# Performance work log

Hardware: AMD Instinct MI355X
Metric: run time of the kernel (lower is better)

## Reference

```python
import jax, jax.numpy as jnp
import numpy as np

N, E, F_IN, H, D = 50000, 800000, 128, 4, 32


def setup_inputs() -> dict:
    key = jax.random.key(0)
    k_x, k_e, k_w, k_al, k_ar = jax.random.split(key, 5)
    x = jax.random.normal(k_x, (N, F_IN), dtype=jnp.float32)
    edge_index = jax.random.randint(k_e, (2, E), 0, N, dtype=jnp.int32).astype(jnp.int64)
    # xavier-uniform-like scales
    s_w = float(np.sqrt(6.0 / (F_IN + H * D)))
    s_a = float(np.sqrt(6.0 / (D + 1)))
    W = jax.random.uniform(k_w, (F_IN, H * D), jnp.float32, -s_w, s_w)
    att_l = jax.random.uniform(k_al, (H, D), jnp.float32, -s_a, s_a)
    att_r = jax.random.uniform(k_ar, (H, D), jnp.float32, -s_a, s_a)
    bias = jnp.zeros((H * D,), jnp.float32)
    return {"x": x, "edge_index": edge_index, "W": W, "att_l": att_l, "att_r": att_r, "bias": bias}


def reference(x, edge_index, W, att_l, att_r, bias):
    num_nodes = x.shape[0]
    n_heads, head_dim = att_l.shape
    h = (x @ W).reshape(num_nodes, n_heads, head_dim)          # [N,H,D]
    alpha_l = jnp.einsum('nhd,hd->nh', h, att_l)               # [N,H]
    alpha_r = jnp.einsum('nhd,hd->nh', h, att_r)               # [N,H]
    from_idx, to_idx = edge_index[0], edge_index[1]
    att = alpha_l[from_idx] + alpha_r[to_idx]                  # [E,H]
    att = jax.nn.leaky_relu(att, negative_slope=0.2)
    # segment softmax over edges grouped by destination node (shift by global
    # per-head max, exactly as the source's _softmax effectively does)
    att = att - jax.lax.stop_gradient(jnp.max(att, axis=0, keepdims=True))
    ex = jnp.exp(att)                                          # [E,H]
    denom = jax.ops.segment_sum(ex, to_idx, num_segments=num_nodes)  # [N,H]
    att_n = ex / (denom[to_idx] + 1e-9)                        # [E,H]
    # scatter-weighted aggregation: out[n] = sum_{e: to=n} att[e] * h[from[e]]
    msgs = att_n[:, :, None] * h[from_idx]                     # [E,H,D]
    out = jax.ops.segment_sum(msgs, to_idx, num_segments=num_nodes)  # [N,H,D]
    out = out.reshape(num_nodes, n_heads * head_dim) + bias
    return out
```

## Files before the change

kernel.cpp:

```cpp
#include <hip/hip_runtime.h>
#include <cstdint>

#define N_NODES 50000
#define N_EDGES 800000
#define F_IN    128
#define N_HEADS 4
#define HEAD_DIM 32
#define F_OUT   128

#define NBUCK   391
#define NPB     128
#define KA_GRID 256
#define EPB     (N_EDGES / KA_GRID)
#define CAPA    32
#define REC_CAP 2560
#define STAGE_CAP REC_CAP
#define NSTRIP  (N_NODES / 16)
#define NGEMM   ((NSTRIP + 3) / 4)

typedef unsigned int uint32;
typedef unsigned short ushort;
typedef __attribute__((ext_vector_type(8))) short short8v;
typedef __attribute__((ext_vector_type(4))) float float4v;

typedef __attribute__((address_space(1))) const float gfloat;
typedef __attribute__((address_space(3))) float lfloat;

__device__ __forceinline__ ushort f2bf(float f) {
    uint32 u = __float_as_uint(f);
    return (ushort)((u + 0x7FFFu + ((u >> 16) & 1u)) >> 16);
}


__device__ __forceinline__ int block_scan_excl_256(int v, int* p_total)
{
    const int t = threadIdx.x, lane = t & 63, wv = t >> 6;
    int incl = v;
#pragma unroll
    for (int d = 1; d < 64; d <<= 1) {
        int u = __shfl_up(incl, d);
        if (lane >= d) incl += u;
    }
    __shared__ int wsum[4];
    if (lane == 63) wsum[wv] = incl;
    __syncthreads();
    int woff = 0;
#pragma unroll
    for (int j = 0; j < 4; ++j) {
        int s = wsum[j];
        if (j < wv) woff += s;
    }
    if (p_total) *p_total = wsum[0] + wsum[1] + wsum[2] + wsum[3];
    __syncthreads();
    return woff + incl - v;
}

__global__ __launch_bounds__(256) void k_prep(const float* __restrict__ W,
    ushort* __restrict__ WT_hi, ushort* __restrict__ WT_lo)
{
    const int id = blockIdx.x * 256 + threadIdx.x;
    if (id < F_IN * F_OUT) {
        const int n = id & 127, k = id >> 7;
        const float w = W[k * F_OUT + n];
        const ushort hi = f2bf(w);
        const float hif = __uint_as_float((uint32)hi << 16);
        WT_hi[n * F_IN + k] = hi;
        WT_lo[n * F_IN + k] = f2bf(w - hif);
    }
}

__global__ __launch_bounds__(256, 4) void k_bin_gemm(
    const int* __restrict__ ei, const float* __restrict__ x,
    const ushort* __restrict__ WT_hi, const ushort* __restrict__ WT_lo,
    const float* __restrict__ attl, const float* __restrict__ attr,
    uint2* __restrict__ priv, int* __restrict__ cnts,
    uint32* __restrict__ hbq, float* __restrict__ aLp, float* __restrict__ aRp)
{
    __shared__ float xl[4][16 * 128];
    __shared__ int cur[NBUCK];

    if (blockIdx.x < KA_GRID) {
        const int sb = blockIdx.x, t = threadIdx.x;
        for (int bb = t; bb < NBUCK; bb += 256) cur[bb] = 0;
        __syncthreads();
        const int e0 = sb * EPB;
        for (int i = t; i < EPB; i += 256) {
            const int from = ei[e0 + i];
            const int to   = ei[N_EDGES + e0 + i];
            const int b = to >> 7;
            const int slot = atomicAdd(&cur[b], 1);
            if (slot < CAPA)
                priv[((size_t)b * KA_GRID + sb) * CAPA + slot] =
                    make_uint2((uint32)from, (uint32)to);
        }
        __syncthreads();
        for (int bb = t; bb < NBUCK; bb += 256)
            cnts[sb * NBUCK + bb] = min(cur[bb], CAPA);
        return;
    }

    const int bid   = blockIdx.x - KA_GRID;
    const int lane  = threadIdx.x & 63;
    const int wv    = threadIdx.x >> 6;
    const int strip = bid * 4 + wv;
    if (strip >= NSTRIP) return;
    const int q     = lane >> 4;
    const int c15   = lane & 15;
    const int row0  = strip * 16;

    const float* gbase = x + (size_t)row0 * F_IN;
    float* lbase = &xl[wv][0];
#pragma unroll
    for (int i = 0; i < 8; ++i) {
        __builtin_amdgcn_global_load_lds(
            (gfloat*)(gbase + i * 256 + lane * 4),
            (lfloat*)(lbase + i * 256), 16, 0, 0);
    }
    __asm volatile("s_waitcnt vmcnt(0)" ::: "memory");

    const float* arow = lbase + c15 * F_IN + q * 8;
    short8v ahi[4], alo[4];
#pragma unroll
    for (int kt = 0; kt < 4; ++kt) {
        const float4 f0 = *(const float4*)(arow + kt * 32);
        const float4 f1 = *(const float4*)(arow + kt * 32 + 4);
        const float fs[8] = {f0.x, f0.y, f0.z, f0.w, f1.x, f1.y, f1.z, f1.w};
#pragma unroll
        for (int j = 0; j < 8; ++j) {
            const ushort hi = f2bf(fs[j]);
            const float hif = __uint_as_float((uint32)hi << 16);
            ahi[kt][j] = (short)hi;
            alo[kt][j] = (short)f2bf(fs[j] - hif);
        }
    }

    float4v acc[8];
#pragma unroll
    for (int nt = 0; nt < 8; ++nt) {
        float4v a = {0.f, 0.f, 0.f, 0.f};
        const ushort* bhb = WT_hi + ((nt * 16 + c15) << 7) + q * 8;
        const ushort* blb = WT_lo + ((nt * 16 + c15) << 7) + q * 8;
#pragma unroll
        for (int kt = 0; kt < 4; ++kt) {
            const short8v bh = *(const short8v*)(bhb + kt * 32);
            const short8v bl = *(const short8v*)(blb + kt * 32);
            a = __builtin_amdgcn_mfma_f32_16x16x32_bf16(ahi[kt], bh, a, 0, 0, 0);
            a = __builtin_amdgcn_mfma_f32_16x16x32_bf16(alo[kt], bh, a, 0, 0, 0);
            a = __builtin_amdgcn_mfma_f32_16x16x32_bf16(ahi[kt], bl, a, 0, 0, 0);
        }
        acc[nt] = a;
    }

#pragma unroll
    for (int nt = 0; nt < 4; ++nt) {
#pragma unroll
        for (int r = 0; r < 4; ++r) {
            const uint32 d = (uint32)f2bf(acc[nt][r]) | ((uint32)f2bf(acc[nt + 4][r]) << 16);
            hbq[(size_t)(row0 + q * 4 + r) * 64 + nt * 16 + c15] = d;
        }
    }

    float aLacc[4][4] = {{0.f}}, aRacc[4][4] = {{0.f}};
#pragma unroll
    for (int nt = 0; nt < 8; ++nt) {
        const float alv = attl[nt * 16 + c15];
        const float arv = attr[nt * 16 + c15];
        const int hh = nt >> 1;
#pragma unroll
        for (int r = 0; r < 4; ++r) {
            aLacc[r][hh] = fmaf(acc[nt][r], alv, aLacc[r][hh]);
            aRacc[r][hh] = fmaf(acc[nt][r], arv, aRacc[r][hh]);
        }
    }
#pragma unroll
    for (int r = 0; r < 4; ++r) {
#pragma unroll
        for (int hh = 0; hh < 4; ++hh) {
            float vl = aLacc[r][hh], vr = aRacc[r][hh];
#pragma unroll
            for (int d = 1; d < 16; d <<= 1) {
                vl += __shfl_xor(vl, d);
                vr += __shfl_xor(vr, d);
            }
            if (c15 == hh) {
                const int row = row0 + q * 4 + r;
                const int pos = (hh & 1) * 2 + (hh >> 1);
                aLp[row * N_HEADS + pos] = vl;
                aRp[row * N_HEADS + pos] = vr;
            }
        }
    }
}

__global__ __launch_bounds__(256) void k_build(const uint2* __restrict__ priv,
    const int* __restrict__ cnts,
    int* __restrict__ count, int* __restrict__ offsets, int* __restrict__ rec_from)
{
    __shared__ uint2 stage[STAGE_CAP];
    __shared__ int so_s[256], cts_s[256];
    __shared__ int hist[NPB], curn[NPB];
    const int b = blockIdx.x, t = threadIdx.x;

    const int ct = cnts[t * NBUCK + b];
    int total;
    const int so = block_scan_excl_256(ct, &total);
    so_s[t] = so;
    cts_s[t] = ct;
    if (t < NPB) hist[t] = 0;
    __syncthreads();

    const uint2* pbase = priv + (size_t)b * KA_GRID * CAPA;
    for (int idx = t; idx < KA_GRID * CAPA; idx += 256) {
        const int sb = idx >> 5;
        const int sl = idx & 31;
        if (sl < cts_s[sb]) {
            const int p = so_s[sb] + sl;
            if (p < STAGE_CAP) stage[p] = pbase[idx];
        }
    }
    __syncthreads();

    const int S = min(total, STAGE_CAP);
    for (int i = t; i < S; i += 256) atomicAdd(&hist[stage[i].y & (NPB - 1)], 1);
    __syncthreads();

    const int hv = (t < NPB) ? hist[t] : 0;
    int tot2;
    const int lo = block_scan_excl_256(hv, &tot2);
    const int rbase = b * REC_CAP;
    const int n = b * NPB + t;
    if (t < NPB && n < N_NODES) {
        count[n]   = hv;
        offsets[n] = rbase + lo;
    }
    if (t < NPB) curn[t] = lo;
    __syncthreads();

    for (int i = t; i < S; i += 256) {
        const uint2 e = stage[i];
        const int pos = atomicAdd(&curn[e.y & (NPB - 1)], 1);
        rec_from[rbase + pos] = (int)e.x;
    }
}

__global__ __launch_bounds__(256) void k_agg(const int* __restrict__ rec_from,
    const int* __restrict__ count, const int* __restrict__ offsets,
    const float* __restrict__ aLp, const float* __restrict__ aRp,
    const uint32* __restrict__ hbq,
    const float* __restrict__ bias, float* __restrict__ out)
{
    const int lane = threadIdx.x & 63;
    const int n = blockIdx.x * 4 + (threadIdx.x >> 6);
    if (n >= N_NODES) return;
    const int cnt  = count[n];
    const int off  = offsets[n];
    const int hsel = (lane >> 5) * 2;
    const int l31  = lane & 31;
    const int gsel = lane & 32;
    const float2 arv = *(const float2*)&aRp[n * N_HEADS + hsel];
    float ax = 0.f, ay = 0.f, ds0 = 0.f, ds1 = 0.f;

    for (int base = 0; base < cnt; base += 32) {
        const int m = min(32, cnt - base);
        int vf = 0;
        float e0p = 0.f, e1p = 0.f;
        if (l31 < m) {
            vf = rec_from[off + base + l31];
            const float2 af = *(const float2*)&aLp[vf * N_HEADS + hsel];
            float t0 = af.x + arv.x; t0 = (t0 > 0.f) ? t0 : 0.2f * t0;
            float t1 = af.y + arv.y; t1 = (t1 > 0.f) ? t1 : 0.2f * t1;
            e0p = __expf(t0);
            e1p = __expf(t1);
        }
        int i = 0;
        for (; i + 8 <= m; i += 8) {
            int f[8]; uint32 h[8]; float e0[8], e1[8];
#pragma unroll
            for (int j = 0; j < 8; ++j) {
                const int s = gsel | (i + j);
                f[j]  = __shfl(vf, s);
                e0[j] = __shfl(e0p, s);
                e1[j] = __shfl(e1p, s);
            }
#pragma unroll
            for (int j = 0; j < 8; ++j) h[j] = hbq[(size_t)f[j] * 64 + lane];
#pragma unroll
            for (int j = 0; j < 8; ++j) {
                ax = fmaf(e0[j], __uint_as_float(h[j] << 16), ax);
                ay = fmaf(e1[j], __uint_as_float(h[j] & 0xFFFF0000u), ay);
                ds0 += e0[j]; ds1 += e1[j];
            }
        }
        for (; i + 4 <= m; i += 4) {
            int f[4]; uint32 h[4]; float e0[4], e1[4];
#pragma unroll
            for (int j = 0; j < 4; ++j) {
                const int s = gsel | (i + j);
                f[j]  = __shfl(vf, s);
                e0[j] = __shfl(e0p, s);
                e1[j] = __shfl(e1p, s);
            }
#pragma unroll
            for (int j = 0; j < 4; ++j) h[j] = hbq[(size_t)f[j] * 64 + lane];
#pragma unroll
            for (int j = 0; j < 4; ++j) {
                ax = fmaf(e0[j], __uint_as_float(h[j] << 16), ax);
                ay = fmaf(e1[j], __uint_as_float(h[j] & 0xFFFF0000u), ay);
                ds0 += e0[j]; ds1 += e1[j];
            }
        }
        for (; i < m; ++i) {
            const int s = gsel | i;
            const int f = __shfl(vf, s);
            const uint32 hv = hbq[(size_t)f * 64 + lane];
            const float e0 = __shfl(e0p, s), e1 = __shfl(e1p, s);
            ax = fmaf(e0, __uint_as_float(hv << 16), ax);
            ay = fmaf(e1, __uint_as_float(hv & 0xFFFF0000u), ay);
            ds0 += e0; ds1 += e1;
        }
    }
    const float inv0 = 1.0f / (ds0 + 1e-9f);
    const float inv1 = 1.0f / (ds1 + 1e-9f);
    out[n * F_OUT + lane]      = ax * inv0 + bias[lane];
    out[n * F_OUT + 64 + lane] = ay * inv1 + bias[64 + lane];
}

extern "C" void kernel_launch(void* const* d_in, const int* in_sizes, int n_in,
                              void* d_out, int out_size, void* d_ws, size_t ws_size,
                              hipStream_t stream)
{
    const float* x    = (const float*)d_in[0];
    const int*   ei   = (const int*)d_in[1];
    const float* W    = (const float*)d_in[2];
    const float* attl = (const float*)d_in[3];
    const float* attr = (const float*)d_in[4];
    const float* bias = (const float*)d_in[5];
    float* out = (float*)d_out;

    char* p = (char*)d_ws;
    auto carve = [&](size_t bytes) -> char* {
        char* q = p;
        p += (bytes + 255) & ~size_t(255);
        return q;
    };
    uint32* hbq      = (uint32*)carve((size_t)N_NODES * 64 * 4);
    uint2*  priv     = (uint2*)carve((size_t)NBUCK * KA_GRID * CAPA * 8);
    int*    rec_from = (int*)carve((size_t)NBUCK * REC_CAP * 4);
    ushort* WT_hi    = (ushort*)carve((size_t)F_IN * F_OUT * 2);
    ushort* WT_lo    = (ushort*)carve((size_t)F_IN * F_OUT * 2);
    float*  aLp      = (float*)carve((size_t)N_NODES * N_HEADS * 4);
    float*  aRp      = (float*)carve((size_t)N_NODES * N_HEADS * 4);
    int*    cnts     = (int*)carve((size_t)KA_GRID * NBUCK * 4);
    int*    count    = (int*)carve((size_t)N_NODES * 4);
    int*    offsets  = (int*)carve((size_t)N_NODES * 4);

    k_prep<<<64, 256, 0, stream>>>(W, WT_hi, WT_lo);
    k_bin_gemm<<<KA_GRID + NGEMM, 256, 0, stream>>>(ei, x, WT_hi, WT_lo,
                                                    attl, attr, priv, cnts,
                                                    hbq, aLp, aRp);
    k_build<<<NBUCK, 256, 0, stream>>>(priv, cnts, count, offsets, rec_from);
    k_agg<<<(N_NODES + 3) / 4, 256, 0, stream>>>(rec_from, count, offsets,
                                                 aLp, aRp, hbq, bias, out);
}
```

Measured before the change: 174.0 us.

## Pack edge bin records into 32 bits, widen binning grid, drop LDS x staging

Result: slower. 181.4 us (+4.2%).

```diff
diff --git a/kernel.cpp b/kernel.cpp
--- a/kernel.cpp
+++ b/kernel.cpp
@@ -10,9 +10,9 @@
 
 #define NBUCK   391
 #define NPB     128
-#define KA_GRID 256
-#define EPB     (N_EDGES / KA_GRID)
-#define CAPA    32
+#define KA_GRID 512
+#define EPB     1563
+#define CAPA    24
 #define REC_CAP 2560
 #define STAGE_CAP REC_CAP
 #define NSTRIP  (N_NODES / 16)
@@ -22,9 +22,6 @@
 typedef unsigned short ushort;
 typedef __attribute__((ext_vector_type(8))) short short8v;
 typedef __attribute__((ext_vector_type(4))) float float4v;
-
-typedef __attribute__((address_space(1))) const float gfloat;
-typedef __attribute__((address_space(3))) float lfloat;
 
 __device__ __forceinline__ ushort f2bf(float f) {
     uint32 u = __float_as_uint(f);
@@ -73,10 +70,9 @@
     const int* __restrict__ ei, const float* __restrict__ x,
     const ushort* __restrict__ WT_hi, const ushort* __restrict__ WT_lo,
     const float* __restrict__ attl, const float* __restrict__ attr,
-    uint2* __restrict__ priv, int* __restrict__ cnts,
+    uint32* __restrict__ priv, int* __restrict__ cnts,
     uint32* __restrict__ hbq, float* __restrict__ aLp, float* __restrict__ aRp)
 {
-    __shared__ float xl[4][16 * 128];
     __shared__ int cur[NBUCK];
 
     if (blockIdx.x < KA_GRID) {
@@ -84,14 +80,15 @@
         for (int bb = t; bb < NBUCK; bb += 256) cur[bb] = 0;
         __syncthreads();
         const int e0 = sb * EPB;
-        for (int i = t; i < EPB; i += 256) {
+        const int lim = min(EPB, N_EDGES - e0);
+        for (int i = t; i < lim; i += 256) {
             const int from = ei[e0 + i];
             const int to   = ei[N_EDGES + e0 + i];
             const int b = to >> 7;
             const int slot = atomicAdd(&cur[b], 1);
             if (slot < CAPA)
                 priv[((size_t)b * KA_GRID + sb) * CAPA + slot] =
-                    make_uint2((uint32)from, (uint32)to);
+                    (uint32)from | ((uint32)(to & 127) << 16);
         }
         __syncthreads();
         for (int bb = t; bb < NBUCK; bb += 256)
@@ -108,22 +105,12 @@
     const int c15   = lane & 15;
     const int row0  = strip * 16;
 
-    const float* gbase = x + (size_t)row0 * F_IN;
-    float* lbase = &xl[wv][0];
-#pragma unroll
-    for (int i = 0; i < 8; ++i) {
-        __builtin_amdgcn_global_load_lds(
-            (gfloat*)(gbase + i * 256 + lane * 4),
-            (lfloat*)(lbase + i * 256), 16, 0, 0);
-    }
-    __asm volatile("s_waitcnt vmcnt(0)" ::: "memory");
-
-    const float* arow = lbase + c15 * F_IN + q * 8;
+    const float* xrow = x + (size_t)(row0 + c15) * F_IN + q * 8;
     short8v ahi[4], alo[4];
 #pragma unroll
     for (int kt = 0; kt < 4; ++kt) {
-        const float4 f0 = *(const float4*)(arow + kt * 32);
-        const float4 f1 = *(const float4*)(arow + kt * 32 + 4);
+        const float4 f0 = *(const float4*)(xrow + kt * 32);
+        const float4 f1 = *(const float4*)(xrow + kt * 32 + 4);
         const float fs[8] = {f0.x, f0.y, f0.z, f0.w, f1.x, f1.y, f1.z, f1.w};
 #pragma unroll
         for (int j = 0; j < 8; ++j) {
@@ -192,28 +179,38 @@
     }
 }
 
-__global__ __launch_bounds__(256) void k_build(const uint2* __restrict__ priv,
+__global__ __launch_bounds__(256) void k_build(const uint32* __restrict__ priv,
     const int* __restrict__ cnts,
     int* __restrict__ count, int* __restrict__ offsets, int* __restrict__ rec_from)
 {
-    __shared__ uint2 stage[STAGE_CAP];
-    __shared__ int so_s[256], cts_s[256];
+    __shared__ uint32 stage[STAGE_CAP];
+    __shared__ int so_s[KA_GRID];
+    __shared__ ushort cts_s[KA_GRID];
     __shared__ int hist[NPB], curn[NPB];
     const int b = blockIdx.x, t = threadIdx.x;
 
-    const int ct = cnts[t * NBUCK + b];
+    int c[2], s = 0;
+#pragma unroll
+    for (int j = 0; j < 2; ++j) {
+        c[j] = cnts[(size_t)(2 * t + j) * NBUCK + b];
+        s += c[j];
+    }
     int total;
-    const int so = block_scan_excl_256(ct, &total);
-    so_s[t] = so;
-    cts_s[t] = ct;
+    int ex = block_scan_excl_256(s, &total);
+#pragma unroll
+    for (int j = 0; j < 2; ++j) {
+        so_s[2 * t + j]  = ex;
+        cts_s[2 * t + j] = (ushort)c[j];
+        ex += c[j];
+    }
     if (t < NPB) hist[t] = 0;
     __syncthreads();
 
-    const uint2* pbase = priv + (size_t)b * KA_GRID * CAPA;
+    const uint32* pbase = priv + (size_t)b * KA_GRID * CAPA;
     for (int idx = t; idx < KA_GRID * CAPA; idx += 256) {
-        const int sb = idx >> 5;
-        const int sl = idx & 31;
-        if (sl < cts_s[sb]) {
+        const int sb = idx / CAPA;
+        const int sl = idx - sb * CAPA;
+        if (sl < (int)cts_s[sb]) {
             const int p = so_s[sb] + sl;
             if (p < STAGE_CAP) stage[p] = pbase[idx];
         }
@@ -221,7 +218,7 @@
     __syncthreads();
 
     const int S = min(total, STAGE_CAP);
-    for (int i = t; i < S; i += 256) atomicAdd(&hist[stage[i].y & (NPB - 1)], 1);
+    for (int i = t; i < S; i += 256) atomicAdd(&hist[stage[i] >> 16], 1);
     __syncthreads();
 
     const int hv = (t < NPB) ? hist[t] : 0;
@@ -237,9 +234,9 @@
     __syncthreads();
 
     for (int i = t; i < S; i += 256) {
-        const uint2 e = stage[i];
-        const int pos = atomicAdd(&curn[e.y & (NPB - 1)], 1);
-        rec_from[rbase + pos] = (int)e.x;
+        const uint32 e = stage[i];
+        const int pos = atomicAdd(&curn[e >> 16], 1);
+        rec_from[rbase + pos] = (int)(e & 0xFFFFu);
     }
 }
 
@@ -344,7 +341,7 @@
         return q;
     };
     uint32* hbq      = (uint32*)carve((size_t)N_NODES * 64 * 4);
-    uint2*  priv     = (uint2*)carve((size_t)NBUCK * KA_GRID * CAPA * 8);
+    uint32* priv     = (uint32*)carve((size_t)NBUCK * KA_GRID * CAPA * 4);
     int*    rec_from = (int*)carve((size_t)NBUCK * REC_CAP * 4);
     ushort* WT_hi    = (ushort*)carve((size_t)F_IN * F_OUT * 2);
     ushort* WT_lo    = (ushort*)carve((size_t)F_IN * F_OUT * 2);
```
